# Kernel tuning notes

Measured on AMD Instinct MI355X. Metric: run time of the kernel, lower is better.

Reference implementation:

```python
import jax, jax.numpy as jnp
import numpy as np

N_USERS = 100000
N_ITEMS = 50000
N_LAYERS = 3
LATENT_DIM = 64
N_INTERACTIONS = 600000
BATCH = 4096
N_TOTAL = N_USERS + N_ITEMS


def setup_inputs() -> dict:
    key = jax.random.key(0)
    k_e, k_u, k_p, k_n = jax.random.split(key, 4)

    # --- build bipartite interaction graph (numpy, host-side like scipy in the original) ---
    rng = np.random.default_rng(0)
    u = rng.integers(0, N_USERS, size=N_INTERACTIONS)
    i = rng.integers(0, N_ITEMS, size=N_INTERACTIONS) + N_USERS
    # symmetrize: A[u, i] = 1 and A[i, u] = 1
    row = np.concatenate([u, i]).astype(np.int32)
    col = np.concatenate([i, u]).astype(np.int32)
    # symmetric degree normalization: D^{-1/2} A D^{-1/2}
    deg = np.bincount(row, minlength=N_TOTAL).astype(np.float32)
    d_inv = np.power(deg + 1e-9, -0.5)
    d_inv[np.isinf(d_inv)] = 0.0
    vals = (d_inv[row] * d_inv[col]).astype(np.float32)

    # Xavier-uniform init for E0 (fan_in = fan_out = dims of the weight matrix)
    limit = float(np.sqrt(6.0 / (N_TOTAL + LATENT_DIM)))
    E0 = jax.random.uniform(k_e, (N_TOTAL, LATENT_DIM), jnp.float32, -limit, limit)

    return {
        "users": jax.random.randint(k_u, (BATCH,), 0, N_USERS),
        "pos_items": jax.random.randint(k_p, (BATCH,), 0, N_ITEMS),
        "neg_items": jax.random.randint(k_n, (BATCH,), 0, N_ITEMS),
        "E0": E0,
        "adj_row": jnp.asarray(row),
        "adj_col": jnp.asarray(col),
        "adj_vals": jnp.asarray(vals),
    }


def reference(users, pos_items, neg_items, E0, adj_row, adj_col, adj_vals):
    # SpMM via gather + segment-sum: out[r] = sum_{e: row[e]=r} vals[e] * E[col[e]]
    def spmm(E):
        return jax.ops.segment_sum(adj_vals[:, None] * E[adj_col], adj_row,
                                   num_segments=N_TOTAL)

    # layer propagation with running sum (mean over layer stack)
    E_k = E0
    acc = E0
    for _ in range(N_LAYERS):
        E_k = spmm(E_k)
        acc = acc + E_k
    final_emb = acc / (N_LAYERS + 1)  # [N_TOTAL, D]

    user_emb = final_emb[:N_USERS]
    item_emb = final_emb[N_USERS:]

    u_emb = user_emb[users]
    pos_emb = item_emb[pos_items]
    neg_emb = item_emb[neg_items]
    u_emb0 = E0[users]
    pos_emb0 = E0[N_USERS + pos_items]
    neg_emb0 = E0[N_USERS + neg_items]
    return (u_emb, pos_emb, neg_emb, u_emb0, pos_emb0, neg_emb0)
```

## Files before the change

kernel.cpp:

```cpp
#include <hip/hip_runtime.h>
#include <hip/hip_fp16.h>

#define LATENT 64
#define N_USERS_C 100000

#define BROWS 128
#define LOG_BROWS 7
#define NBUCK_MAX 1280
#define NBLKA_MAX 512
#define SORT_T 256
#define SORT_E 16
#define SORT_CHUNK (SORT_T * SORT_E)
#define BUCK_CAP 4608

typedef unsigned short ushort8_t __attribute__((ext_vector_type(8)));

__device__ __forceinline__ unsigned enc_val14(float v) {
    unsigned vb = (unsigned)__float_as_int(v) + 0x1000u;
    return (((vb >> 23) - 0x77u) << 10) | ((vb >> 13) & 0x3FFu);
}
__device__ __forceinline__ float dec_val14(unsigned m) {
    return __uint_as_float(m ? ((((m >> 10) + 0x77u) << 23) | ((m & 0x3FFu) << 13)) : 0u);
}


__global__ void sortA_conv_kernel(const int* __restrict__ row, const int* __restrict__ col,
                                  const float* __restrict__ vals,
                                  unsigned* __restrict__ aux, unsigned char* __restrict__ rowloc,
                                  int* __restrict__ cntmat, int* __restrict__ srcmat,
                                  int* __restrict__ bcnt, int nnz, int nbuck, int nblkA,
                                  const float* __restrict__ E0, __half* __restrict__ E0h,
                                  int n4) {
    __shared__ int cnt[NBUCK_MAX];
    __shared__ int off[NBUCK_MAX];
    __shared__ int part[SORT_T];
    __shared__ unsigned buf[SORT_CHUNK];
    __shared__ unsigned char rbuf[SORT_CHUNK];
    int t = threadIdx.x;

    if (blockIdx.x >= nblkA) {
        int cb = blockIdx.x - nblkA;
        int base4 = cb * (SORT_T * 4);
#pragma unroll
        for (int jj = 0; jj < 4; jj++) {
            int i = base4 + jj * SORT_T + t;
            if (i < n4) {
                float4 v = ((const float4*)E0)[i];
                __half2* o = (__half2*)E0h;
                o[2 * i]     = __floats2half2_rn(v.x, v.y);
                o[2 * i + 1] = __floats2half2_rn(v.z, v.w);
            }
        }
        return;
    }

    int blk = blockIdx.x;
    int base = blk * SORT_CHUNK;

    for (int i = t; i < nbuck; i += SORT_T) cnt[i] = 0;
    __syncthreads();

    int      eb[SORT_E];
    unsigned pl[SORT_E];
    unsigned char rl8[SORT_E];
    int quadbase = base >> 2;
#pragma unroll
    for (int jq = 0; jq < SORT_E / 4; jq++) {
        int q = quadbase + jq * SORT_T + t;
        int e0 = 4 * q;
        if (e0 + 3 < nnz) {
            int4   r4 = ((const int4*)row)[q];
            int4   c4 = ((const int4*)col)[q];
            float4 v4 = ((const float4*)vals)[q];
            int   rr[4] = { r4.x, r4.y, r4.z, r4.w };
            int   cc[4] = { c4.x, c4.y, c4.z, c4.w };
            float vv[4] = { v4.x, v4.y, v4.z, v4.w };
#pragma unroll
            for (int jj = 0; jj < 4; jj++) {
                int j = 4 * jq + jj;
                int r = rr[jj];
                int b = r >> LOG_BROWS;
                eb[j] = b;
                pl[j] = (unsigned)cc[jj] | (enc_val14(vv[jj]) << 18);
                rl8[j] = (unsigned char)(r & (BROWS - 1));
                atomicAdd(&cnt[b], 1);
            }
        } else {
#pragma unroll
            for (int jj = 0; jj < 4; jj++) {
                int j = 4 * jq + jj;
                int e = e0 + jj;
                if (e < nnz) {
                    int r = row[e];
                    int b = r >> LOG_BROWS;
                    eb[j] = b;
                    pl[j] = (unsigned)col[e] | (enc_val14(vals[e]) << 18);
                    rl8[j] = (unsigned char)(r & (BROWS - 1));
                    atomicAdd(&cnt[b], 1);
                } else {
                    eb[j] = -1;
                }
            }
        }
    }
    __syncthreads();

    int chunk = (nbuck + SORT_T - 1) / SORT_T;
    int lo = t * chunk, hi = lo + chunk; if (hi > nbuck) hi = nbuck;
    int s = 0;
    for (int i = lo; i < hi; i++) s += cnt[i];
    part[t] = s;
    __syncthreads();
    for (int o = 1; o < SORT_T; o <<= 1) {
        int x = (t >= o) ? part[t - o] : 0;
        __syncthreads();
        part[t] += x;
        __syncthreads();
    }
    int run = (t == 0) ? 0 : part[t - 1];
    for (int i = lo; i < hi; i++) { off[i] = run; run += cnt[i]; }
    __syncthreads();

#pragma unroll
    for (int j = 0; j < SORT_E; j++) {
        if (eb[j] >= 0) {
            int p = atomicAdd(&off[eb[j]], 1);
            buf[p] = pl[j];
            rbuf[p] = rl8[j];
        }
    }
    __syncthreads();

    for (int b = t; b < nbuck; b += SORT_T) {
        int c = cnt[b];
        int beg = off[b] - c;
        cntmat[(size_t)blk * nbuck + b] = c;
        srcmat[(size_t)blk * nbuck + b] = beg;
        if (c) atomicAdd(&bcnt[b], c);
    }
    int nvalid = nnz - base; if (nvalid > SORT_CHUNK) nvalid = SORT_CHUNK;
    for (int i = t; i < nvalid; i += SORT_T) {
        aux[base + i] = buf[i];
        rowloc[base + i] = rbuf[i];
    }
}


__global__ void sortB_spmm1_kernel(const unsigned* __restrict__ aux,
                                   const unsigned char* __restrict__ rowloc,
                                   const int* __restrict__ cntmat, const int* __restrict__ srcmat,
                                   const int* __restrict__ bcnt,
                                   unsigned* __restrict__ edges, int* __restrict__ startOut,
                                   int* __restrict__ origRow, int* __restrict__ slotOfRow,
                                   const __half* __restrict__ E0h, __half* __restrict__ E1,
                                   int nblkA, int nbuck, int ntotal, int nnz) {
    __shared__ int rs[NBLKA_MAX], roff[NBLKA_MAX + 1];
    __shared__ int part[SORT_T];
    __shared__ unsigned buf[BUCK_CAP];
    __shared__ unsigned char rbuf[BUCK_CAP];
    __shared__ int cnt128[BROWS];
    __shared__ int slotOf[BROWS];
    __shared__ int rowOf[BROWS];
    __shared__ int offS[BROWS];
    __shared__ int placeOff[BROWS];
    __shared__ int dhist[64];
    int b = blockIdx.x, t = threadIdx.x;

    int sb = 0;
    for (int i = t; i < b; i += SORT_T) sb += bcnt[i];
    part[t] = sb;
    __syncthreads();
    for (int o = 1; o < SORT_T; o <<= 1) {
        int x = (t >= o) ? part[t - o] : 0;
        __syncthreads();
        part[t] += x;
        __syncthreads();
    }
    int base = part[SORT_T - 1];
    int tot = bcnt[b];
    __syncthreads();

    int rbase = b * BROWS;
    int nr = ntotal - rbase; if (nr > BROWS) nr = BROWS;

    int chunk = (nblkA + SORT_T - 1) / SORT_T;
    int lo = t * chunk, hi = lo + chunk; if (hi > nblkA) hi = nblkA;
    int rcl[8];
    int s = 0;
    for (int i = lo; i < hi; i++) {
        int c = cntmat[(size_t)i * nbuck + b];
        rcl[i - lo] = c;
        rs[i] = srcmat[(size_t)i * nbuck + b];
        s += c;
    }
    part[t] = s;
    if (t < BROWS) cnt128[t] = 0;
    if (t < 64) dhist[t] = 0;
    __syncthreads();
    for (int o = 1; o < SORT_T; o <<= 1) {
        int x = (t >= o) ? part[t - o] : 0;
        __syncthreads();
        part[t] += x;
        __syncthreads();
    }
    int run = (t == 0) ? 0 : part[t - 1];
    for (int i = lo; i < hi; i++) { roff[i] = run; run += rcl[i - lo]; }
    if (t == SORT_T - 1) roff[nblkA] = part[SORT_T - 1];
    __syncthreads();

    for (int i = t; i < tot; i += SORT_T) {
        int lo2 = 0, hi2 = nblkA;
        while (hi2 - lo2 > 1) {
            int mid = (lo2 + hi2) >> 1;
            if (roff[mid] <= i) lo2 = mid; else hi2 = mid;
        }
        size_t src = (size_t)lo2 * SORT_CHUNK + rs[lo2] + (i - roff[lo2]);
        buf[i] = aux[src];
        unsigned char rl = rowloc[src];
        rbuf[i] = rl;
        atomicAdd(&cnt128[rl], 1);
    }
    __syncthreads();

    if (t < nr) { int d = min(cnt128[t], 63); atomicAdd(&dhist[d], 1); }
    __syncthreads();
    part[t] = (t < 64) ? dhist[t] : 0;
    __syncthreads();
    for (int o = 1; o < 64; o <<= 1) {
        int x = (t >= o) ? part[t - o] : 0;
        __syncthreads();
        part[t] += x;
        __syncthreads();
    }
    if (t < 64) dhist[t] = (t == 0) ? 0 : part[t - 1];
    __syncthreads();
    if (t < nr) {
        int d = min(cnt128[t], 63);
        int sl = atomicAdd(&dhist[d], 1);
        slotOf[t] = sl;
        rowOf[sl] = t;
    }
    __syncthreads();

    part[t] = (t < nr) ? cnt128[rowOf[t]] : 0;
    __syncthreads();
    for (int o = 1; o < SORT_T; o <<= 1) {
        int x = (t >= o) ? part[t - o] : 0;
        __syncthreads();
        part[t] += x;
        __syncthreads();
    }
    if (t < nr) offS[t] = (t == 0) ? 0 : part[t - 1];
    __syncthreads();

    if (t < nr) {
        startOut[rbase + t]   = base + offS[t];
        origRow[rbase + t]    = rbase + rowOf[t];
        slotOfRow[rbase + t]  = rbase + slotOf[t];
        placeOff[t] = offS[slotOf[t]];
    }
    if (b == nbuck - 1 && t == 0) startOut[ntotal] = nnz;
    __syncthreads();

    for (int i = t; i < tot; i += SORT_T) {
        int p = atomicAdd(&placeOff[rbuf[i]], 1);
        edges[base + p] = buf[i];
    }
    __syncthreads();

    {
        int wv = t >> 6;
        int lane = t & 63;
        int g = lane >> 3, l = lane & 7;
        for (int sl = 8 * wv + g; sl < nr; sl += 32) {
            int bb = base + offS[sl];
            int ee = bb + cnt128[rowOf[sl]];
            int ro = rbase + rowOf[sl];
            float a0 = 0.f, a1 = 0.f, a2 = 0.f, a3 = 0.f;
            float a4 = 0.f, a5 = 0.f, a6 = 0.f, a7 = 0.f;
            for (int k = (bb & ~3); k < ee; k += 4) {
                uint4 ev = *(const uint4*)(edges + k);
                unsigned ed[4] = { ev.x, ev.y, ev.z, ev.w };
#pragma unroll
                for (int j = 0; j < 4; j++) {
                    int kk = k + j;
                    if (kk < bb || kk >= ee) ed[j] = 0u;
                }
                ushort8_t gv[4];
#pragma unroll
                for (int j = 0; j < 4; j++) {
                    gv[j] = *(const ushort8_t*)(E0h + (size_t)(ed[j] & 0x3FFFFu) * LATENT + 8 * l);
                }
#pragma unroll
                for (int j = 0; j < 4; j++) {
                    float wv2 = dec_val14(ed[j] >> 18);
                    const __half2* h2 = (const __half2*)&gv[j];
                    a0 += wv2 * __low2float(h2[0]);
                    a1 += wv2 * __high2float(h2[0]);
                    a2 += wv2 * __low2float(h2[1]);
                    a3 += wv2 * __high2float(h2[1]);
                    a4 += wv2 * __low2float(h2[2]);
                    a5 += wv2 * __high2float(h2[2]);
                    a6 += wv2 * __low2float(h2[3]);
                    a7 += wv2 * __high2float(h2[3]);
                }
            }
            union { ushort8_t u; __half2 h[4]; } o;
            o.h[0] = __floats2half2_rn(a0, a1);
            o.h[1] = __floats2half2_rn(a2, a3);
            o.h[2] = __floats2half2_rn(a4, a5);
            o.h[3] = __floats2half2_rn(a6, a7);
            *(ushort8_t*)(E1 + (size_t)ro * LATENT + 8 * l) = o.u;
        }
    }
}


__global__ void spmm_slot(const int* __restrict__ start, const int* __restrict__ origRow,
                          const unsigned* __restrict__ edges,
                          const __half* __restrict__ Ein, __half* __restrict__ Eout,
                          int nslots) {
    int t = blockIdx.x * blockDim.x + threadIdx.x;
    int w = t >> 6;
    int lane = t & 63;
    int g = lane >> 3, l = lane & 7;
    int s = 8 * w + g;
    if (s >= nslots) return;
    int b = start[s];
    int e = start[s + 1];
    int ro = origRow[s];
    float a0 = 0.f, a1 = 0.f, a2 = 0.f, a3 = 0.f;
    float a4 = 0.f, a5 = 0.f, a6 = 0.f, a7 = 0.f;
    for (int k = (b & ~3); k < e; k += 4) {
        uint4 ev = *(const uint4*)(edges + k);
        unsigned ed[4] = { ev.x, ev.y, ev.z, ev.w };
#pragma unroll
        for (int j = 0; j < 4; j++) {
            int kk = k + j;
            if (kk < b || kk >= e) ed[j] = 0u;
        }
        ushort8_t gv[4];
#pragma unroll
        for (int j = 0; j < 4; j++) {
            gv[j] = *(const ushort8_t*)(Ein + (size_t)(ed[j] & 0x3FFFFu) * LATENT + 8 * l);
        }
#pragma unroll
        for (int j = 0; j < 4; j++) {
            float wv = dec_val14(ed[j] >> 18);
            const __half2* h2 = (const __half2*)&gv[j];
            a0 += wv * __low2float(h2[0]);
            a1 += wv * __high2float(h2[0]);
            a2 += wv * __low2float(h2[1]);
            a3 += wv * __high2float(h2[1]);
            a4 += wv * __low2float(h2[2]);
            a5 += wv * __high2float(h2[2]);
            a6 += wv * __low2float(h2[3]);
            a7 += wv * __high2float(h2[3]);
        }
    }
    union { ushort8_t u; __half2 h[4]; } o;
    o.h[0] = __floats2half2_rn(a0, a1);
    o.h[1] = __floats2half2_rn(a2, a3);
    o.h[2] = __floats2half2_rn(a4, a5);
    o.h[3] = __floats2half2_rn(a6, a7);
    *(ushort8_t*)(Eout + (size_t)ro * LATENT + 8 * l) = o.u;
}


__global__ void fin_fused(const int* __restrict__ users, const int* __restrict__ pos,
                          const int* __restrict__ neg,
                          const int* __restrict__ start, const int* __restrict__ slotOfRow,
                          const unsigned* __restrict__ edges,
                          const float* __restrict__ E0, const __half* __restrict__ E1,
                          const __half* __restrict__ E2,
                          float* __restrict__ out, int batch) {
    int t = blockIdx.x * blockDim.x + threadIdx.x;
    int w = t >> 6;
    int lane = t & 63;
    int g = lane >> 4, l = lane & 15;
    int i = 4 * w + g;
    int nent = 3 * batch;
    if (i >= nent) return;
    int grp = i / batch;
    int bb = i - grp * batch;
    int r = (grp == 0) ? users[bb] : (grp == 1) ? (N_USERS_C + pos[bb]) : (N_USERS_C + neg[bb]);
    int s = slotOfRow[r];
    int b = start[s];
    int e = start[s + 1];
    float a0 = 0.f, a1 = 0.f, a2 = 0.f, a3 = 0.f;
    for (int k = (b & ~3); k < e; k += 4) {
        uint4 ev = *(const uint4*)(edges + k);
        unsigned ed[4] = { ev.x, ev.y, ev.z, ev.w };
#pragma unroll
        for (int j = 0; j < 4; j++) {
            int kk = k + j;
            if (kk < b || kk >= e) ed[j] = 0u;
        }
        ushort4 gv[4];
#pragma unroll
        for (int j = 0; j < 4; j++) {
            gv[j] = *(const ushort4*)(E2 + (size_t)(ed[j] & 0x3FFFFu) * LATENT + 4 * l);
        }
#pragma unroll
        for (int j = 0; j < 4; j++) {
            float wv = dec_val14(ed[j] >> 18);
            const __half2* h2 = (const __half2*)&gv[j];
            a0 += wv * __low2float(h2[0]);
            a1 += wv * __high2float(h2[0]);
            a2 += wv * __low2float(h2[1]);
            a3 += wv * __high2float(h2[1]);
        }
    }
    size_t idx = (size_t)r * LATENT + 4 * l;
    float4 e0v = *(const float4*)(E0 + idx);
    ushort4 e1u = *(const ushort4*)(E1 + idx);
    ushort4 e2u = *(const ushort4*)(E2 + idx);
    const __half2* h1 = (const __half2*)&e1u;
    const __half2* h2v = (const __half2*)&e2u;
    float4 res;
    res.x = 0.25f * (e0v.x + __low2float(h1[0])  + __low2float(h2v[0])  + a0);
    res.y = 0.25f * (e0v.y + __high2float(h1[0]) + __high2float(h2v[0]) + a1);
    res.z = 0.25f * (e0v.z + __low2float(h1[1])  + __low2float(h2v[1])  + a2);
    res.w = 0.25f * (e0v.w + __high2float(h1[1]) + __high2float(h2v[1]) + a3);
    int total = nent * LATENT;
    *(float4*)(out + (size_t)i * LATENT + 4 * l) = res;
    *(float4*)(out + total + (size_t)i * LATENT + 4 * l) = e0v;
}

extern "C" void kernel_launch(void* const* d_in, const int* in_sizes, int n_in,
                              void* d_out, int out_size, void* d_ws, size_t ws_size,
                              hipStream_t stream) {
    const int*   users = (const int*)d_in[0];
    const int*   pos   = (const int*)d_in[1];
    const int*   neg   = (const int*)d_in[2];
    const float* E0    = (const float*)d_in[3];
    const int*   row   = (const int*)d_in[4];
    const int*   col   = (const int*)d_in[5];
    const float* vals  = (const float*)d_in[6];
    float*       out   = (float*)d_out;

    const int batch  = in_sizes[0];
    const int nnz    = in_sizes[4];
    const int ntotal = in_sizes[3] / LATENT;
    const int nbuck  = (ntotal + BROWS - 1) / BROWS;
    const int nblkA  = (nnz + SORT_CHUNK - 1) / SORT_CHUNK;

    auto align256 = [](size_t x) { return (x + 255) & ~(size_t)255; };

    const size_t hbufBytes = align256((size_t)ntotal * LATENT * sizeof(__half));
    const size_t edgeBytes = align256((size_t)nnz * sizeof(unsigned) + 16);
    const size_t auxBytes  = align256((size_t)nnz * sizeof(unsigned));
    const size_t matBytes  = align256((size_t)nblkA * nbuck * sizeof(int));
    const size_t stBytes   = align256((size_t)(ntotal + 1) * sizeof(int));
    const size_t bsBytes   = align256((size_t)(nbuck + 1) * sizeof(int));

    char* p = (char*)d_ws;
    __half* E0h      = (__half*)p;          p += hbufBytes;
    __half* bufA     = (__half*)p;          p += hbufBytes;
    __half* bufB     = (__half*)p;          p += hbufBytes;
    __half* bufC     = (__half*)p;          p += hbufBytes;
    unsigned* edges  = (unsigned*)p;        p += edgeBytes;
    int*    startA   = (int*)p;             p += stBytes;
    int*    origRow  = (int*)p;             p += stBytes;
    int*    slotOfRw = (int*)p;             p += stBytes;
    int*    bcnt     = (int*)p;             p += bsBytes;
    unsigned*      aux    = (unsigned*)bufC;
    unsigned char* rowloc = (unsigned char*)((char*)bufC + auxBytes);
    int* cntmat = (int*)bufB;
    int* srcmat = (int*)((char*)bufB + matBytes);

    hipMemsetAsync(bcnt, 0, (size_t)nbuck * sizeof(int), stream);

    const int threads = 256;
    const int slotWaves = (ntotal + 7) / 8;
    const int spBlocks = (slotWaves * 64 + threads - 1) / threads;
    const int nent = 3 * batch;
    const int fBlocks = (((nent + 3) / 4) * 64 + threads - 1) / threads;
    const int n4 = ntotal * LATENT / 4;
    const int cBlocks4 = (n4 + SORT_T * 4 - 1) / (SORT_T * 4);

    sortA_conv_kernel<<<nblkA + cBlocks4, SORT_T, 0, stream>>>(
        row, col, vals, aux, rowloc, cntmat, srcmat, bcnt, nnz, nbuck, nblkA,
        E0, E0h, n4);
    sortB_spmm1_kernel<<<nbuck, SORT_T, 0, stream>>>(aux, rowloc, cntmat, srcmat, bcnt,
                                                     edges, startA, origRow, slotOfRw,
                                                     E0h, bufA,
                                                     nblkA, nbuck, ntotal, nnz);

    spmm_slot<<<spBlocks, threads, 0, stream>>>(startA, origRow, edges, bufA, bufB, ntotal);
    fin_fused<<<fBlocks, threads, 0, stream>>>(users, pos, neg, startA, slotOfRw, edges,
                                               E0, bufA, bufB, out, batch);
}
```

Baseline: 181.3 us.

## Halve sort bucket size, pack count/offset matrix, use wave-shuffle scans

Shrinks the row bucket from 128 to 64 rows, which doubles the number of sortB blocks and cuts per-block shared memory so more blocks can run concurrently. The separate count and source-offset matrices are packed into one 32-bit word (16-bit offset, 16-bit count), halving that matrix traffic. The shared-memory Hillis-Steele scans with many barriers are replaced by wave-level shuffle scans plus a small cross-wave combine. In exchange, sortA has a larger per-block bucket histogram, and the 16-bit packing and BUCK_CAP of 1536 depend on per-bucket counts staying within those limits.

Result: no change. 179.0 us (-1.3%).

```diff
diff --git a/kernel.cpp b/kernel.cpp
--- a/kernel.cpp
+++ b/kernel.cpp
@@ -4,14 +4,14 @@
 #define LATENT 64
 #define N_USERS_C 100000
 
-#define BROWS 128
-#define LOG_BROWS 7
-#define NBUCK_MAX 1280
+#define BROWS 64
+#define LOG_BROWS 6
+#define NBUCK_MAX 2368
 #define NBLKA_MAX 512
 #define SORT_T 256
 #define SORT_E 16
 #define SORT_CHUNK (SORT_T * SORT_E)
-#define BUCK_CAP 4608
+#define BUCK_CAP 1536
 
 typedef unsigned short ushort8_t __attribute__((ext_vector_type(8)));
 
@@ -23,17 +23,37 @@
     return __uint_as_float(m ? ((((m >> 10) + 0x77u) << 23) | ((m & 0x3FFu) << 13)) : 0u);
 }
 
+__device__ __forceinline__ int wave_iscan(int x, int lane) {
+#pragma unroll
+    for (int o = 1; o < 64; o <<= 1) {
+        int y = __shfl_up(x, o, 64);
+        if (lane >= o) x += y;
+    }
+    return x;
+}
+__device__ __forceinline__ int block_escan(int v, int* ws, int* tot) {
+    int t = threadIdx.x, lane = t & 63, w = t >> 6;
+    int inc = wave_iscan(v, lane);
+    __syncthreads();
+    if (lane == 63) ws[w] = inc;
+    __syncthreads();
+    int s0 = ws[0], s1 = ws[1], s2 = ws[2], s3 = ws[3];
+    *tot = s0 + s1 + s2 + s3;
+    int base = (w > 0 ? s0 : 0) + (w > 1 ? s1 : 0) + (w > 2 ? s2 : 0);
+    return base + inc - v;
+}
+
 
 __global__ void sortA_conv_kernel(const int* __restrict__ row, const int* __restrict__ col,
                                   const float* __restrict__ vals,
                                   unsigned* __restrict__ aux, unsigned char* __restrict__ rowloc,
-                                  int* __restrict__ cntmat, int* __restrict__ srcmat,
+                                  unsigned* __restrict__ csmat,
                                   int* __restrict__ bcnt, int nnz, int nbuck, int nblkA,
                                   const float* __restrict__ E0, __half* __restrict__ E0h,
                                   int n4) {
     __shared__ int cnt[NBUCK_MAX];
     __shared__ int off[NBUCK_MAX];
-    __shared__ int part[SORT_T];
+    __shared__ int ws[4];
     __shared__ unsigned buf[SORT_CHUNK];
     __shared__ unsigned char rbuf[SORT_CHUNK];
     int t = threadIdx.x;
@@ -109,15 +129,8 @@
     int lo = t * chunk, hi = lo + chunk; if (hi > nbuck) hi = nbuck;
     int s = 0;
     for (int i = lo; i < hi; i++) s += cnt[i];
-    part[t] = s;
-    __syncthreads();
-    for (int o = 1; o < SORT_T; o <<= 1) {
-        int x = (t >= o) ? part[t - o] : 0;
-        __syncthreads();
-        part[t] += x;
-        __syncthreads();
-    }
-    int run = (t == 0) ? 0 : part[t - 1];
+    int tot_;
+    int run = block_escan(s, ws, &tot_);
     for (int i = lo; i < hi; i++) { off[i] = run; run += cnt[i]; }
     __syncthreads();
 
@@ -134,8 +147,7 @@
     for (int b = t; b < nbuck; b += SORT_T) {
         int c = cnt[b];
         int beg = off[b] - c;
-        cntmat[(size_t)blk * nbuck + b] = c;
-        srcmat[(size_t)blk * nbuck + b] = beg;
+        csmat[(size_t)blk * nbuck + b] = ((unsigned)beg << 16) | (unsigned)c;
         if (c) atomicAdd(&bcnt[b], c);
     }
     int nvalid = nnz - base; if (nvalid > SORT_CHUNK) nvalid = SORT_CHUNK;
@@ -148,64 +160,51 @@
 
 __global__ void sortB_spmm1_kernel(const unsigned* __restrict__ aux,
                                    const unsigned char* __restrict__ rowloc,
-                                   const int* __restrict__ cntmat, const int* __restrict__ srcmat,
+                                   const unsigned* __restrict__ csmat,
                                    const int* __restrict__ bcnt,
                                    unsigned* __restrict__ edges, int* __restrict__ startOut,
                                    int* __restrict__ origRow, int* __restrict__ slotOfRow,
                                    const __half* __restrict__ E0h, __half* __restrict__ E1,
                                    int nblkA, int nbuck, int ntotal, int nnz) {
     __shared__ int rs[NBLKA_MAX], roff[NBLKA_MAX + 1];
-    __shared__ int part[SORT_T];
+    __shared__ int ws[4];
     __shared__ unsigned buf[BUCK_CAP];
     __shared__ unsigned char rbuf[BUCK_CAP];
-    __shared__ int cnt128[BROWS];
+    __shared__ int cnt64[BROWS];
     __shared__ int slotOf[BROWS];
     __shared__ int rowOf[BROWS];
     __shared__ int offS[BROWS];
     __shared__ int placeOff[BROWS];
     __shared__ int dhist[64];
     int b = blockIdx.x, t = threadIdx.x;
+    int lane = t & 63;
 
     int sb = 0;
     for (int i = t; i < b; i += SORT_T) sb += bcnt[i];
-    part[t] = sb;
-    __syncthreads();
-    for (int o = 1; o < SORT_T; o <<= 1) {
-        int x = (t >= o) ? part[t - o] : 0;
-        __syncthreads();
-        part[t] += x;
-        __syncthreads();
-    }
-    int base = part[SORT_T - 1];
+    int base;
+    (void)block_escan(sb, ws, &base);
     int tot = bcnt[b];
-    __syncthreads();
 
     int rbase = b * BROWS;
     int nr = ntotal - rbase; if (nr > BROWS) nr = BROWS;
 
     int chunk = (nblkA + SORT_T - 1) / SORT_T;
     int lo = t * chunk, hi = lo + chunk; if (hi > nblkA) hi = nblkA;
-    int rcl[8];
+    int rcl[2];
     int s = 0;
     for (int i = lo; i < hi; i++) {
-        int c = cntmat[(size_t)i * nbuck + b];
+        unsigned v = csmat[(size_t)i * nbuck + b];
+        int c = (int)(v & 0xFFFFu);
         rcl[i - lo] = c;
-        rs[i] = srcmat[(size_t)i * nbuck + b];
+        rs[i] = (int)(v >> 16);
         s += c;
     }
-    part[t] = s;
-    if (t < BROWS) cnt128[t] = 0;
+    if (t < BROWS) cnt64[t] = 0;
     if (t < 64) dhist[t] = 0;
-    __syncthreads();
-    for (int o = 1; o < SORT_T; o <<= 1) {
-        int x = (t >= o) ? part[t - o] : 0;
-        __syncthreads();
-        part[t] += x;
-        __syncthreads();
-    }
-    int run = (t == 0) ? 0 : part[t - 1];
+    int totE;
+    int run = block_escan(s, ws, &totE);
     for (int i = lo; i < hi; i++) { roff[i] = run; run += rcl[i - lo]; }
-    if (t == SORT_T - 1) roff[nblkA] = part[SORT_T - 1];
+    if (t == 0) roff[nblkA] = totE;
     __syncthreads();
 
     for (int i = t; i < tot; i += SORT_T) {
@@ -218,39 +217,30 @@
         buf[i] = aux[src];
         unsigned char rl = rowloc[src];
         rbuf[i] = rl;
-        atomicAdd(&cnt128[rl], 1);
-    }
-    __syncthreads();
-
-    if (t < nr) { int d = min(cnt128[t], 63); atomicAdd(&dhist[d], 1); }
-    __syncthreads();
-    part[t] = (t < 64) ? dhist[t] : 0;
-    __syncthreads();
-    for (int o = 1; o < 64; o <<= 1) {
-        int x = (t >= o) ? part[t - o] : 0;
-        __syncthreads();
-        part[t] += x;
-        __syncthreads();
-    }
-    if (t < 64) dhist[t] = (t == 0) ? 0 : part[t - 1];
+        atomicAdd(&cnt64[rl], 1);
+    }
+    __syncthreads();
+
+    if (t < nr) { int d = min(cnt64[t], 63); atomicAdd(&dhist[d], 1); }
+    __syncthreads();
+    if (t < 64) {
+        int x = dhist[lane];
+        int inc = wave_iscan(x, lane);
+        dhist[lane] = inc - x;
+    }
     __syncthreads();
     if (t < nr) {
-        int d = min(cnt128[t], 63);
+        int d = min(cnt64[t], 63);
         int sl = atomicAdd(&dhist[d], 1);
         slotOf[t] = sl;
         rowOf[sl] = t;
     }
     __syncthreads();
-
-    part[t] = (t < nr) ? cnt128[rowOf[t]] : 0;
-    __syncthreads();
-    for (int o = 1; o < SORT_T; o <<= 1) {
-        int x = (t >= o) ? part[t - o] : 0;
-        __syncthreads();
-        part[t] += x;
-        __syncthreads();
-    }
-    if (t < nr) offS[t] = (t == 0) ? 0 : part[t - 1];
+    if (t < 64) {
+        int x = (lane < nr) ? cnt64[rowOf[lane]] : 0;
+        int inc = wave_iscan(x, lane);
+        offS[lane] = inc - x;
+    }
     __syncthreads();
 
     if (t < nr) {
@@ -270,11 +260,10 @@
 
     {
         int wv = t >> 6;
-        int lane = t & 63;
         int g = lane >> 3, l = lane & 7;
         for (int sl = 8 * wv + g; sl < nr; sl += 32) {
             int bb = base + offS[sl];
-            int ee = bb + cnt128[rowOf[sl]];
+            int ee = bb + cnt64[rowOf[sl]];
             int ro = rbase + rowOf[sl];
             float a0 = 0.f, a1 = 0.f, a2 = 0.f, a3 = 0.f;
             float a4 = 0.f, a5 = 0.f, a6 = 0.f, a7 = 0.f;
@@ -450,7 +439,6 @@
     const size_t hbufBytes = align256((size_t)ntotal * LATENT * sizeof(__half));
     const size_t edgeBytes = align256((size_t)nnz * sizeof(unsigned) + 16);
     const size_t auxBytes  = align256((size_t)nnz * sizeof(unsigned));
-    const size_t matBytes  = align256((size_t)nblkA * nbuck * sizeof(int));
     const size_t stBytes   = align256((size_t)(ntotal + 1) * sizeof(int));
     const size_t bsBytes   = align256((size_t)(nbuck + 1) * sizeof(int));
 
@@ -466,8 +454,7 @@
     int*    bcnt     = (int*)p;             p += bsBytes;
     unsigned*      aux    = (unsigned*)bufC;
     unsigned char* rowloc = (unsigned char*)((char*)bufC + auxBytes);
-    int* cntmat = (int*)bufB;
-    int* srcmat = (int*)((char*)bufB + matBytes);
+    unsigned* csmat = (unsigned*)bufB;
 
     hipMemsetAsync(bcnt, 0, (size_t)nbuck * sizeof(int), stream);
 
@@ -480,9 +467,9 @@
     const int cBlocks4 = (n4 + SORT_T * 4 - 1) / (SORT_T * 4);
 
     sortA_conv_kernel<<<nblkA + cBlocks4, SORT_T, 0, stream>>>(
-        row, col, vals, aux, rowloc, cntmat, srcmat, bcnt, nnz, nbuck, nblkA,
+        row, col, vals, aux, rowloc, csmat, bcnt, nnz, nbuck, nblkA,
         E0, E0h, n4);
-    sortB_spmm1_kernel<<<nbuck, SORT_T, 0, stream>>>(aux, rowloc, cntmat, srcmat, bcnt,
+    sortB_spmm1_kernel<<<nbuck, SORT_T, 0, stream>>>(aux, rowloc, csmat, bcnt,
                                                      edges, startA, origRow, slotOfRw,
                                                      E0h, bufA,
                                                      nblkA, nbuck, ntotal, nnz);
```
